# Kernel tuning notes

Measured on AMD Instinct MI355X. Metric: run time of the kernel, lower is better.

Reference implementation:

```python
import jax, jax.numpy as jnp
import numpy as np

S = 14
L_COORD = 5.0
L_NOOBJ = 0.5
EPS = 1e-20


def _corners(box):
    # box: (..., 5) with [x, y, w, h, c]; convert center/size -> corner coords (per torch code)
    xc = box[..., 0] / S
    yc = box[..., 1] / S
    x1 = xc - 0.5 * box[..., 2]
    y1 = yc - 0.5 * box[..., 3]
    x2 = xc + 0.5 * box[..., 2]
    y2 = yc + 0.5 * box[..., 3]
    return x1, y1, x2, y2


def _pairwise_diag_iou(bt, bp):
    # bt, bp: (..., 5). Torch builds an NxM IoU matrix and takes the diagonal;
    # the diagonal is just the elementwise (row-wise) IoU, computed here directly.
    tx1, ty1, tx2, ty2 = _corners(bt)
    px1, py1, px2, py2 = _corners(bp)
    iw = jnp.maximum(jnp.minimum(tx2, px2) - jnp.maximum(tx1, px1), 0.0)
    ih = jnp.maximum(jnp.minimum(ty2, py2) - jnp.maximum(ty1, py1), 0.0)
    inter = iw * ih
    area_t = (tx2 - tx1) * (ty2 - ty1)
    area_p = (px2 - px1) * (py2 - py1)
    return inter / (area_t + area_p - inter)


def yolo_loss(pred, tgt):
    N = pred.shape[0]
    dt = pred.dtype

    obj = (tgt[..., 4] + tgt[..., 9]) > 0            # (N,S,S) cells containing an object
    objf = obj.astype(dt)
    noobjf = 1.0 - objf

    # --- no-object loss: confidences (ch 4 and 9) of no-object cells ---
    no_object_loss = jnp.sum(
        noobjf * ((pred[..., 4] - tgt[..., 4]) ** 2 + (pred[..., 9] - tgt[..., 9]) ** 2)
    )

    # --- class loss over object cells ---
    class_loss = jnp.sum(objf * jnp.sum((pred[..., 10:30] - tgt[..., 10:30]) ** 2, axis=-1))

    # --- per-cell box pairs ---
    bp = pred[..., :10].reshape(pred.shape[:3] + (2, 5))   # (N,S,S,2,5)
    bt = tgt[..., :10].reshape(tgt.shape[:3] + (2, 5))

    iou = jax.lax.stop_gradient(_pairwise_diag_iou(bt, bp))  # (N,S,S,2); detached in torch

    # Responsible-box selection, faithfully replicating the torch stride-2 trick:
    # a[::2] = iou0 > iou1 ; a[1::2] = float(a[::2]) <= iou1
    iou0, iou1 = iou[..., 0], iou[..., 1]
    a0 = iou0 > iou1
    a1 = a0.astype(dt) <= iou1
    sel = jnp.stack([a0, a1], axis=-1).astype(dt)          # (N,S,S,2)
    w = objf[..., None] * sel                              # response weight per box

    # --- containing-object confidence loss (target = detached IoU) ---
    contain_loss = jnp.sum(w * (bp[..., 4] - iou) ** 2)

    dx = bp[..., 0] - bt[..., 0]
    dy = bp[..., 1] - bt[..., 1]
    dsw = jnp.sqrt(bp[..., 2] + EPS) - jnp.sqrt(bt[..., 2] + EPS)
    dsh = jnp.sqrt(bp[..., 3] + EPS) - jnp.sqrt(bt[..., 3] + EPS)
    regression_loss = jnp.sum(w * (dx ** 2 + dy ** 2 + dsw ** 2 + dsh ** 2))

    total = (L_COORD * regression_loss + contain_loss
             + L_NOOBJ * no_object_loss + class_loss) / N
    return total


def setup_inputs() -> dict:
    key = jax.random.key(0)
    k1, k2, k3 = jax.random.split(key, 3)
    N = 4096
    pred = jax.random.uniform(k1, (N, S, S, 30), dtype=jnp.float32)
    tgt = jax.random.uniform(k2, (N, S, S, 30), dtype=jnp.float32)
    obj_cell = (jax.random.uniform(k3, (N, S, S)) < 0.05).astype(jnp.float32)
    tgt = tgt.at[..., 4].multiply(obj_cell)
    tgt = tgt.at[..., 9].multiply(obj_cell)
    return {"pred_tensor": pred, "target_tensor": tgt}


def reference(pred_tensor, target_tensor):
    return yolo_loss(pred_tensor, target_tensor)
```

## Files before the change

### kernel.cpp

```cpp
#include <hip/hip_runtime.h>

namespace {
constexpr int   S_GRID   = 14;
constexpr int   CH       = 30;
constexpr float L_COORD  = 5.0f;
constexpr float L_NOOBJ  = 0.5f;
constexpr float BOX_EPS  = 1e-20f;
constexpr int   BLOCK    = 256;
constexpr int   TILE     = 256;
}

__global__ __launch_bounds__(BLOCK) void yolo_loss_kernel(
    const float* __restrict__ pred,
    const float* __restrict__ tgt,
    float* __restrict__ out,
    float inv_n)
{
    __shared__ float sp[TILE * CH];
    __shared__ float st[TILE * CH];
    __shared__ float wsum[BLOCK / 64];

    const int tid = threadIdx.x;
    const size_t base = (size_t)blockIdx.x * (TILE * CH);

    const float4* gp4 = reinterpret_cast<const float4*>(pred + base);
    const float4* gt4 = reinterpret_cast<const float4*>(tgt + base);
    float4* sp4 = reinterpret_cast<float4*>(sp);
    float4* st4 = reinterpret_cast<float4*>(st);
    constexpr int NV4 = TILE * CH / 4;
    #pragma unroll
    for (int i = 0; i < (NV4 + BLOCK - 1) / BLOCK; ++i) {
        int idx = tid + i * BLOCK;
        if (idx < NV4) {
            sp4[idx] = gp4[idx];
            st4[idx] = gt4[idx];
        }
    }
    __syncthreads();

    const float* p = sp + tid * CH;
    const float* t = st + tid * CH;
    float pv[CH], tv[CH];
    #pragma unroll
    for (int j = 0; j < CH / 2; ++j) {
        float2 a = reinterpret_cast<const float2*>(p)[j];
        pv[2 * j] = a.x; pv[2 * j + 1] = a.y;
        float2 b = reinterpret_cast<const float2*>(t)[j];
        tv[2 * j] = b.x; tv[2 * j + 1] = b.y;
    }

    const float objf   = ((tv[4] + tv[9]) > 0.0f) ? 1.0f : 0.0f;
    const float noobjf = 1.0f - objf;

    const float d4 = pv[4] - tv[4];
    const float d9 = pv[9] - tv[9];
    const float no_obj = noobjf * (d4 * d4 + d9 * d9);

    float cls = 0.0f;
    #pragma unroll
    for (int j = 10; j < CH; ++j) {
        const float d = pv[j] - tv[j];
        cls += d * d;
    }
    cls *= objf;

    float iou[2];
    constexpr float invS = 1.0f / (float)S_GRID;
    #pragma unroll
    for (int b = 0; b < 2; ++b) {
        const float* bp = pv + 5 * b;
        const float* bt = tv + 5 * b;
        const float txc = bt[0] * invS, tyc = bt[1] * invS;
        const float tx1 = txc - 0.5f * bt[2], tx2 = txc + 0.5f * bt[2];
        const float ty1 = tyc - 0.5f * bt[3], ty2 = tyc + 0.5f * bt[3];
        const float pxc = bp[0] * invS, pyc = bp[1] * invS;
        const float px1 = pxc - 0.5f * bp[2], px2 = pxc + 0.5f * bp[2];
        const float py1 = pyc - 0.5f * bp[3], py2 = pyc + 0.5f * bp[3];
        const float iw = fmaxf(fminf(tx2, px2) - fmaxf(tx1, px1), 0.0f);
        const float ih = fmaxf(fminf(ty2, py2) - fmaxf(ty1, py1), 0.0f);
        const float inter  = iw * ih;
        const float area_t = (tx2 - tx1) * (ty2 - ty1);
        const float area_p = (px2 - px1) * (py2 - py1);
        iou[b] = inter / (area_t + area_p - inter);
    }

    const bool  a0   = iou[0] > iou[1];
    const bool  a1   = (a0 ? 1.0f : 0.0f) <= iou[1];
    const float sel0 = a0 ? 1.0f : 0.0f;
    const float sel1 = a1 ? 1.0f : 0.0f;

    float contain = 0.0f, regr = 0.0f;
    #pragma unroll
    for (int b = 0; b < 2; ++b) {
        const float w  = objf * (b == 0 ? sel0 : sel1);
        const float* bp = pv + 5 * b;
        const float* bt = tv + 5 * b;
        const float dc = bp[4] - iou[b];
        contain += w * dc * dc;
        const float dx  = bp[0] - bt[0];
        const float dy  = bp[1] - bt[1];
        const float dsw = sqrtf(bp[2] + BOX_EPS) - sqrtf(bt[2] + BOX_EPS);
        const float dsh = sqrtf(bp[3] + BOX_EPS) - sqrtf(bt[3] + BOX_EPS);
        regr += w * (dx * dx + dy * dy + dsw * dsw + dsh * dsh);
    }

    float acc = L_COORD * regr + contain + L_NOOBJ * no_obj + cls;

    #pragma unroll
    for (int off = 32; off > 0; off >>= 1)
        acc += __shfl_down(acc, off, 64);
    const int lane = tid & 63;
    const int wid  = tid >> 6;
    if (lane == 0) wsum[wid] = acc;
    __syncthreads();
    if (tid == 0) {
        const float s = (wsum[0] + wsum[1]) + (wsum[2] + wsum[3]);
        atomicAdd(out, s * inv_n);
    }
}

extern "C" void kernel_launch(void* const* d_in, const int* in_sizes, int n_in,
                              void* d_out, int out_size, void* d_ws, size_t ws_size,
                              hipStream_t stream) {
    const float* pred = (const float*)d_in[0];
    const float* tgt  = (const float*)d_in[1];
    float* out = (float*)d_out;

    const int ncells = in_sizes[0] / CH;
    const int n_batch = ncells / (S_GRID * S_GRID);
    const int grid = ncells / TILE;

    hipMemsetAsync(out, 0, sizeof(float), stream);
    yolo_loss_kernel<<<grid, BLOCK, 0, stream>>>(pred, tgt, out,
                                                 1.0f / (float)n_batch);
}
```

Baseline: 210.6 us.

## Load cells directly from global memory and spread atomics over padded slots

Drops the shared-memory staging: each thread now reads its own 30-float cell straight from global memory as float2 loads. It also replaces the single global atomic with atomics spread across 256 cache-line-padded slots, summed by a small finalize kernel. The goal is to lift the LDS occupancy limit (about 61KB per block before) and to remove contention on one atomic address. The cost is uncoalesced strided global loads, since each thread reads 120 contiguous bytes, plus an extra kernel launch.

```diff
diff --git a/kernel.cpp b/kernel.cpp
--- a/kernel.cpp
+++ b/kernel.cpp
@@ -7,39 +7,23 @@
 constexpr float L_NOOBJ  = 0.5f;
 constexpr float BOX_EPS  = 1e-20f;
 constexpr int   BLOCK    = 256;
-constexpr int   TILE     = 256;
+constexpr int   NSLOT    = 256;
+constexpr int   SLOT_STRIDE = 16;
 }
 
-__global__ __launch_bounds__(BLOCK) void yolo_loss_kernel(
+__global__ __launch_bounds__(BLOCK) void yolo_main_kernel(
     const float* __restrict__ pred,
     const float* __restrict__ tgt,
-    float* __restrict__ out,
-    float inv_n)
+    float* __restrict__ partial)
 {
-    __shared__ float sp[TILE * CH];
-    __shared__ float st[TILE * CH];
     __shared__ float wsum[BLOCK / 64];
 
-    const int tid = threadIdx.x;
-    const size_t base = (size_t)blockIdx.x * (TILE * CH);
+    const int tid  = threadIdx.x;
+    const size_t cell = (size_t)blockIdx.x * BLOCK + tid;
 
-    const float4* gp4 = reinterpret_cast<const float4*>(pred + base);
-    const float4* gt4 = reinterpret_cast<const float4*>(tgt + base);
-    float4* sp4 = reinterpret_cast<float4*>(sp);
-    float4* st4 = reinterpret_cast<float4*>(st);
-    constexpr int NV4 = TILE * CH / 4;
-    #pragma unroll
-    for (int i = 0; i < (NV4 + BLOCK - 1) / BLOCK; ++i) {
-        int idx = tid + i * BLOCK;
-        if (idx < NV4) {
-            sp4[idx] = gp4[idx];
-            st4[idx] = gt4[idx];
-        }
-    }
-    __syncthreads();
+    const float* p = pred + cell * CH;
+    const float* t = tgt  + cell * CH;
 
-    const float* p = sp + tid * CH;
-    const float* t = st + tid * CH;
     float pv[CH], tv[CH];
     #pragma unroll
     for (int j = 0; j < CH / 2; ++j) {
@@ -115,8 +99,27 @@
     __syncthreads();
     if (tid == 0) {
         const float s = (wsum[0] + wsum[1]) + (wsum[2] + wsum[3]);
-        atomicAdd(out, s * inv_n);
+        atomicAdd(&partial[(blockIdx.x & (NSLOT - 1)) * SLOT_STRIDE], s);
     }
+}
+
+__global__ __launch_bounds__(NSLOT) void yolo_finalize_kernel(
+    const float* __restrict__ partial,
+    float* __restrict__ out,
+    float inv_n)
+{
+    __shared__ float wsum[NSLOT / 64];
+    const int tid = threadIdx.x;
+    float v = partial[tid * SLOT_STRIDE];
+    #pragma unroll
+    for (int off = 32; off > 0; off >>= 1)
+        v += __shfl_down(v, off, 64);
+    const int lane = tid & 63;
+    const int wid  = tid >> 6;
+    if (lane == 0) wsum[wid] = v;
+    __syncthreads();
+    if (tid == 0)
+        out[0] = ((wsum[0] + wsum[1]) + (wsum[2] + wsum[3])) * inv_n;
 }
 
 extern "C" void kernel_launch(void* const* d_in, const int* in_sizes, int n_in,
@@ -124,13 +127,15 @@
                               hipStream_t stream) {
     const float* pred = (const float*)d_in[0];
     const float* tgt  = (const float*)d_in[1];
-    float* out = (float*)d_out;
+    float* out     = (float*)d_out;
+    float* partial = (float*)d_ws;
 
-    const int ncells = in_sizes[0] / CH;
+    const int ncells  = in_sizes[0] / CH;
     const int n_batch = ncells / (S_GRID * S_GRID);
-    const int grid = ncells / TILE;
+    const int grid    = ncells / BLOCK;
 
-    hipMemsetAsync(out, 0, sizeof(float), stream);
-    yolo_loss_kernel<<<grid, BLOCK, 0, stream>>>(pred, tgt, out,
-                                                 1.0f / (float)n_batch);
+    hipMemsetAsync(partial, 0, NSLOT * SLOT_STRIDE * sizeof(float), stream);
+    yolo_main_kernel<<<grid, BLOCK, 0, stream>>>(pred, tgt, partial);
+    yolo_finalize_kernel<<<1, NSLOT, 0, stream>>>(partial, out,
+                                                  1.0f / (float)n_batch);
 }
```

New measurement: 210.8 us. No clear change (+0.1%).
